# Kernel tuning notes

Hardware: AMD Instinct MI355X
Metric: run time of the kernel (lower is better)

The kernel has to match this reference:

```python
import jax, jax.numpy as jnp
import numpy as np

N = 50000        # nodes
E = 150000       # edges (avg degree ~3, chain-like RNA graphs)
F_IN = 32        # n_features
H = 32           # hidden_dim
C = 13           # n_classes
L = 3            # n_conv_layers
EDGE_HID = 10    # edge-net hidden width (Linear(2,10))
BN_EPS = 1e-5
SLOPE = 0.01     # leaky_relu default negative slope


def setup_inputs() -> dict:
    key = jax.random.key(0)
    ks = jax.random.split(key, 8)
    s = 0.1
    x = jax.random.normal(ks[0], (N, F_IN), dtype=jnp.float32)
    edge_index = jax.random.randint(ks[1], (2, E), 0, N)
    edge_attr = jax.random.uniform(ks[2], (E, 2), dtype=jnp.float32)
    # per-layer NNConv params stacked on a leading L axis (F_IN == H so all layers share shapes)
    netW1 = jax.random.normal(ks[3], (L, 2, EDGE_HID), dtype=jnp.float32) * s
    netb1 = jnp.zeros((L, EDGE_HID), dtype=jnp.float32)
    netW2 = jax.random.normal(ks[4], (L, EDGE_HID, F_IN * H), dtype=jnp.float32) * (s / np.sqrt(EDGE_HID).astype(np.float32))
    netb2 = jnp.zeros((L, F_IN * H), dtype=jnp.float32)
    root = jax.random.normal(ks[5], (L, F_IN, H), dtype=jnp.float32) * s
    conv_bias = jnp.zeros((L, H), dtype=jnp.float32)
    bn_gamma = jnp.ones((L, H), dtype=jnp.float32)
    bn_beta = jnp.zeros((L, H), dtype=jnp.float32)
    fcW = jax.random.normal(ks[6], (H, C), dtype=jnp.float32) * s
    fcb = jnp.zeros((C,), dtype=jnp.float32)
    return {"x": x, "edge_index": edge_index, "edge_attr": edge_attr,
            "netW1": netW1, "netb1": netb1, "netW2": netW2, "netb2": netb2,
            "root": root, "conv_bias": conv_bias,
            "bn_gamma": bn_gamma, "bn_beta": bn_beta, "fcW": fcW, "fcb": fcb}


def reference(x, edge_index, edge_attr, netW1, netb1, netW2, netb2, root,
              conv_bias, bn_gamma, bn_beta, fcW, fcb):
    src, dst = edge_index[0], edge_index[1]
    n = x.shape[0]
    h = x
    for i in range(L):
        # NNConv: per-edge weight matrix from edge MLP
        e = jax.nn.relu(edge_attr @ netW1[i] + netb1[i])            # [E, EDGE_HID]
        w = (e @ netW2[i] + netb2[i]).reshape(-1, h.shape[1], H)    # [E, in, H]
        m = jnp.einsum('ei,eio->eo', h[src], w)                     # messages [E, H]
        agg = jax.ops.segment_sum(m, dst, num_segments=n)           # scatter-add to targets
        h = agg + h @ root[i] + conv_bias[i]
        # BatchNorm1d (training-mode batch statistics)
        mu = h.mean(axis=0)
        var = h.var(axis=0)
        h = (h - mu) * jax.lax.rsqrt(var + BN_EPS) * bn_gamma[i] + bn_beta[i]
        # leaky_relu; dropout=0 is identity
        h = jnp.where(h > 0, h, SLOPE * h)
    logits = h @ fcW + fcb
    return jax.nn.log_softmax(logits, axis=1)
```

## Files before the change

kernel.cpp:

```cpp
#include <hip/hip_runtime.h>

#define NN 50000
#define EE 150000
#define BN_EPS 1e-5f
#define SLOPE 0.01f
#define SCAN_B 196
#define AGG_B  1563
#define MSG_B  2344

typedef __attribute__((ext_vector_type(8))) short bf16x8;
typedef __attribute__((ext_vector_type(4))) float f32x4;

__global__ __launch_bounds__(256) void k_count(const int* __restrict__ ei, int* __restrict__ cnt) {
    int e = blockIdx.x * blockDim.x + threadIdx.x;
    if (e < EE) atomicAdd(&cnt[ei[EE + e]], 1);
}

__global__ __launch_bounds__(256) void k_scanA(const int* __restrict__ cnt,
                                               int* __restrict__ rowptr,
                                               int* __restrict__ bsum) {
    __shared__ int buf[256];
    int t = threadIdx.x;
    int idx = blockIdx.x * 256 + t;
    int v = (idx <= NN) ? cnt[idx] : 0;
    buf[t] = v;
    __syncthreads();
    for (int off = 1; off < 256; off <<= 1) {
        int add = (t >= off) ? buf[t - off] : 0;
        __syncthreads();
        buf[t] += add;
        __syncthreads();
    }
    if (idx <= NN) rowptr[idx] = buf[t] - v;
    if (t == 255) bsum[blockIdx.x] = buf[255];
}

__global__ __launch_bounds__(256) void k_scanB(int* __restrict__ bsum) {
    __shared__ int buf[256];
    int t = threadIdx.x;
    int v = (t < SCAN_B) ? bsum[t] : 0;
    buf[t] = v;
    __syncthreads();
    for (int off = 1; off < 256; off <<= 1) {
        int add = (t >= off) ? buf[t - off] : 0;
        __syncthreads();
        buf[t] += add;
        __syncthreads();
    }
    if (t < SCAN_B) bsum[t] = buf[t] - v;
}

__global__ __launch_bounds__(256) void k_scanC(int* __restrict__ rowptr,
                                               int* __restrict__ cursor,
                                               const int* __restrict__ bsum) {
    int idx = blockIdx.x * 256 + threadIdx.x;
    if (idx <= NN) {
        int r = rowptr[idx] + bsum[blockIdx.x];
        rowptr[idx] = r;
        cursor[idx] = r;
    }
}

__global__ __launch_bounds__(256) void k_fill(const int* __restrict__ ei,
                                              int* __restrict__ cursor,
                                              int* __restrict__ perm) {
    int e = blockIdx.x * blockDim.x + threadIdx.x;
    if (e < EE) perm[e] = atomicAdd(&cursor[ei[EE + e]], 1);
}

__device__ __forceinline__ void bn_scsh(const float* __restrict__ stats,
                                        const float* __restrict__ gamma,
                                        const float* __restrict__ beta,
                                        int flag, float* sc, float* sh) {
    if (flag && threadIdx.x < 32) {
        int o = threadIdx.x;
        float mu = stats[o] * (1.0f / NN);
        float var = stats[32 + o] * (1.0f / NN) - mu * mu;
        float s = gamma[o] * rsqrtf(var + BN_EPS);
        sc[o] = s;
        sh[o] = fmaf(-mu, s, beta[o]);
    }
}

__global__ __launch_bounds__(256) void k_msg(
    const float* __restrict__ h, const int* __restrict__ ei,
    const float* __restrict__ ea, const float* __restrict__ W1,
    const float* __restrict__ b1, const float* __restrict__ W2,
    const float* __restrict__ b2,
    const float* __restrict__ stats, const float* __restrict__ gamma,
    const float* __restrict__ beta, int flag,
    const int* __restrict__ perm, float* __restrict__ m)
{
    __shared__ unsigned sWu[5632];
    __shared__ float hnF[2048];
    __shared__ float ekL[768];
    __shared__ float sc[32], sh[32];

    int t = threadIdx.x;
    bn_scsh(stats, gamma, beta, flag, sc, sh);
    __syncthreads();

#pragma unroll
    for (int it = 0; it < 22; ++it) {
        int idx = t + 256 * it;
        int frag = idx >> 8;
        int rem  = idx & 255;
        int lane = rem >> 2;
        int j0   = (rem & 3) * 2;
        int tile = frag & 1;
        int kstep = frag >> 1;
        int o  = tile * 16 + (lane & 15);
        int kk = kstep * 32 + (lane >> 4) * 8 + j0;
        float v0, v1;
        if (kk < 320) {
            int base = (kk >> 5) * 1024 + (kk & 31) * 32 + o;
            v0 = W2[base];
            v1 = W2[base + 32];
        } else {
            int base = (kk - 320) * 32 + o;
            v0 = b2[base];
            v1 = b2[base + 32];
        }
        sWu[idx] = __builtin_amdgcn_perm(__float_as_uint(v1), __float_as_uint(v0), 0x07060302u);
    }

    int e_loc = t & 63;
    int c     = t >> 6;
    int e_g   = blockIdx.x * 64 + e_loc;
    bool ev   = e_g < EE;

    if (c == 0) {
        float2 a = ev ? ((const float2*)ea)[e_g] : make_float2(0.f, 0.f);
#pragma unroll
        for (int k = 0; k < 10; ++k)
            ekL[e_loc * 12 + k] = fmaxf(fmaf(a.x, W1[k], fmaf(a.y, W1[10 + k], b1[k])), 0.0f);
        ekL[e_loc * 12 + 10] = 1.0f;
    }

    {
        float4 f0 = make_float4(0.f, 0.f, 0.f, 0.f);
        float4 f1 = make_float4(0.f, 0.f, 0.f, 0.f);
        if (ev) {
            int s = ei[e_g];
            f0 = *(const float4*)(h + s * 32 + c * 8);
            f1 = *(const float4*)(h + s * 32 + c * 8 + 4);
            if (flag) {
                int i0 = c * 8;
                f0.x = fmaf(f0.x, sc[i0+0], sh[i0+0]); f0.x = f0.x > 0.f ? f0.x : SLOPE*f0.x;
                f0.y = fmaf(f0.y, sc[i0+1], sh[i0+1]); f0.y = f0.y > 0.f ? f0.y : SLOPE*f0.y;
                f0.z = fmaf(f0.z, sc[i0+2], sh[i0+2]); f0.z = f0.z > 0.f ? f0.z : SLOPE*f0.z;
                f0.w = fmaf(f0.w, sc[i0+3], sh[i0+3]); f0.w = f0.w > 0.f ? f0.w : SLOPE*f0.w;
                f1.x = fmaf(f1.x, sc[i0+4], sh[i0+4]); f1.x = f1.x > 0.f ? f1.x : SLOPE*f1.x;
                f1.y = fmaf(f1.y, sc[i0+5], sh[i0+5]); f1.y = f1.y > 0.f ? f1.y : SLOPE*f1.y;
                f1.z = fmaf(f1.z, sc[i0+6], sh[i0+6]); f1.z = f1.z > 0.f ? f1.z : SLOPE*f1.z;
                f1.w = fmaf(f1.w, sc[i0+7], sh[i0+7]); f1.w = f1.w > 0.f ? f1.w : SLOPE*f1.w;
            }
        }
        int w = e_loc >> 4;
        int l = (e_loc & 15) + c * 16;
        *(float4*)&hnF[w * 512 + l * 4]       = f0;
        *(float4*)&hnF[w * 512 + 256 + l * 4] = f1;
    }
    __syncthreads();

    int lane = t & 63;
    int w    = t >> 6;
    int el   = w * 16 + (lane & 15);
    f32x4 h0 = *(const f32x4*)&hnF[w * 512 + lane * 4];
    f32x4 h1 = *(const f32x4*)&hnF[w * 512 + 256 + lane * 4];
    float ekv[11];
#pragma unroll
    for (int k = 0; k < 11; ++k) ekv[k] = ekL[el * 12 + k];

    f32x4 acc0 = {0.f, 0.f, 0.f, 0.f};
    f32x4 acc1 = {0.f, 0.f, 0.f, 0.f};
#pragma unroll
    for (int k = 0; k < 11; ++k) {
        float ekk = ekv[k];
        union { unsigned u[4]; bf16x8 v; } B;
        B.u[0] = __builtin_amdgcn_perm(__float_as_uint(ekk * h0.y), __float_as_uint(ekk * h0.x), 0x07060302u);
        B.u[1] = __builtin_amdgcn_perm(__float_as_uint(ekk * h0.w), __float_as_uint(ekk * h0.z), 0x07060302u);
        B.u[2] = __builtin_amdgcn_perm(__float_as_uint(ekk * h1.y), __float_as_uint(ekk * h1.x), 0x07060302u);
        B.u[3] = __builtin_amdgcn_perm(__float_as_uint(ekk * h1.w), __float_as_uint(ekk * h1.z), 0x07060302u);
        bf16x8 A0 = *(const bf16x8*)&sWu[(k * 2)     * 256 + lane * 4];
        bf16x8 A1 = *(const bf16x8*)&sWu[(k * 2 + 1) * 256 + lane * 4];
        acc0 = __builtin_amdgcn_mfma_f32_16x16x32_bf16(A0, B.v, acc0, 0, 0, 0);
        acc1 = __builtin_amdgcn_mfma_f32_16x16x32_bf16(A1, B.v, acc1, 0, 0, 0);
    }

    if (e_g - e_loc + el < EE) {
        int p = perm[blockIdx.x * 64 + el];
        int r = (lane >> 4) * 4;
        *(f32x4*)(m + (size_t)p * 32 + r)      = acc0;
        *(f32x4*)(m + (size_t)p * 32 + 16 + r) = acc1;
    }
}

__global__ __launch_bounds__(256) void k_agg(
    const float* __restrict__ h, const float* __restrict__ m,
    const int* __restrict__ rowptr,
    const float* __restrict__ root, const float* __restrict__ bias,
    const float* __restrict__ stats_prev, const float* __restrict__ gamma,
    const float* __restrict__ beta, int flag,
    float* __restrict__ hpre, float* __restrict__ stats_out)
{
    __shared__ float sc[32], sh[32];
    bn_scsh(stats_prev, gamma, beta, flag, sc, sh);
    __syncthreads();

    int v = blockIdx.x * 32 + (threadIdx.x >> 3);
    int cg = threadIdx.x & 7;
    float4 acc = make_float4(0.f, 0.f, 0.f, 0.f);

    if (v < NN) {
        float hn[32];
        const float4* hp = (const float4*)(h + v * 32);
#pragma unroll
        for (int q = 0; q < 8; ++q) {
            float4 t = hp[q];
            hn[4 * q] = t.x; hn[4 * q + 1] = t.y; hn[4 * q + 2] = t.z; hn[4 * q + 3] = t.w;
        }
        if (flag) {
#pragma unroll
            for (int i = 0; i < 32; ++i) {
                float y = fmaf(hn[i], sc[i], sh[i]);
                hn[i] = y > 0.f ? y : SLOPE * y;
            }
        }
        acc = ((const float4*)bias)[cg];
#pragma unroll
        for (int i = 0; i < 32; ++i) {
            float4 r = ((const float4*)(root + i * 32))[cg];
            acc.x = fmaf(hn[i], r.x, acc.x);
            acc.y = fmaf(hn[i], r.y, acc.y);
            acc.z = fmaf(hn[i], r.z, acc.z);
            acc.w = fmaf(hn[i], r.w, acc.w);
        }
        int q0 = rowptr[v], q1 = rowptr[v + 1];
        float4 acc2 = make_float4(0.f, 0.f, 0.f, 0.f);
        int p = q0;
        for (; p + 1 < q1; p += 2) {
            float4 t0 = ((const float4*)(m + (size_t)p * 32))[cg];
            float4 t1 = ((const float4*)(m + (size_t)(p + 1) * 32))[cg];
            acc.x += t0.x; acc.y += t0.y; acc.z += t0.z; acc.w += t0.w;
            acc2.x += t1.x; acc2.y += t1.y; acc2.z += t1.z; acc2.w += t1.w;
        }
        if (p < q1) {
            float4 t0 = ((const float4*)(m + (size_t)p * 32))[cg];
            acc.x += t0.x; acc.y += t0.y; acc.z += t0.z; acc.w += t0.w;
        }
        acc.x += acc2.x; acc.y += acc2.y; acc.z += acc2.z; acc.w += acc2.w;
        ((float4*)(hpre + v * 32))[cg] = acc;
    }

    float ss[8] = { acc.x, acc.y, acc.z, acc.w,
                    acc.x * acc.x, acc.y * acc.y, acc.z * acc.z, acc.w * acc.w };
#pragma unroll
    for (int d = 8; d < 64; d <<= 1) {
#pragma unroll
        for (int j = 0; j < 8; ++j) ss[j] += __shfl_xor(ss[j], d);
    }
    __shared__ float ls[2][4][8][4];
    int wave = threadIdx.x >> 6, lane = threadIdx.x & 63;
    if (lane < 8) {
#pragma unroll
        for (int j = 0; j < 4; ++j) {
            ls[0][wave][lane][j] = ss[j];
            ls[1][wave][lane][j] = ss[4 + j];
        }
    }
    __syncthreads();
    if (threadIdx.x < 64) {
        int stat = threadIdx.x >> 5, idx = threadIdx.x & 31;
        int cgg = idx >> 2, ch = idx & 3;
        float val = ls[stat][0][cgg][ch] + ls[stat][1][cgg][ch]
                  + ls[stat][2][cgg][ch] + ls[stat][3][cgg][ch];
        unsafeAtomicAdd(&stats_out[stat * 32 + idx], val);
    }
}

__global__ __launch_bounds__(256) void k_logits(const float* __restrict__ h,
                                                const float* __restrict__ fcW,
                                                const float* __restrict__ fcb,
                                                const float* __restrict__ stats,
                                                const float* __restrict__ gamma,
                                                const float* __restrict__ beta,
                                                float* __restrict__ out) {
    __shared__ float sc[32], sh[32];
    bn_scsh(stats, gamma, beta, 1, sc, sh);
    __syncthreads();

    int v = blockIdx.x * blockDim.x + threadIdx.x;
    if (v >= NN) return;
    float hv[32];
    const float4* hp = (const float4*)(h + v * 32);
#pragma unroll
    for (int q = 0; q < 8; ++q) {
        float4 t = hp[q];
        hv[4 * q] = t.x; hv[4 * q + 1] = t.y; hv[4 * q + 2] = t.z; hv[4 * q + 3] = t.w;
    }
#pragma unroll
    for (int i = 0; i < 32; ++i) {
        float y = fmaf(hv[i], sc[i], sh[i]);
        hv[i] = y > 0.f ? y : SLOPE * y;
    }
    float lg[13];
#pragma unroll
    for (int c = 0; c < 13; ++c) lg[c] = fcb[c];
#pragma unroll
    for (int i = 0; i < 32; ++i) {
        float z = hv[i];
#pragma unroll
        for (int c = 0; c < 13; ++c) lg[c] = fmaf(z, fcW[i * 13 + c], lg[c]);
    }
    float mx = lg[0];
#pragma unroll
    for (int c = 1; c < 13; ++c) mx = fmaxf(mx, lg[c]);
    float sum = 0.0f;
#pragma unroll
    for (int c = 0; c < 13; ++c) sum += expf(lg[c] - mx);
    float lse = mx + logf(sum);
#pragma unroll
    for (int c = 0; c < 13; ++c) out[v * 13 + c] = lg[c] - lse;
}

extern "C" void kernel_launch(void* const* d_in, const int* in_sizes, int n_in,
                              void* d_out, int out_size, void* d_ws, size_t ws_size,
                              hipStream_t stream) {
    const float* x     = (const float*)d_in[0];
    const int*   ei    = (const int*)  d_in[1];
    const float* ea    = (const float*)d_in[2];
    const float* netW1 = (const float*)d_in[3];
    const float* netb1 = (const float*)d_in[4];
    const float* netW2 = (const float*)d_in[5];
    const float* netb2 = (const float*)d_in[6];
    const float* root  = (const float*)d_in[7];
    const float* cbias = (const float*)d_in[8];
    const float* gamma = (const float*)d_in[9];
    const float* beta  = (const float*)d_in[10];
    const float* fcW   = (const float*)d_in[11];
    const float* fcb   = (const float*)d_in[12];
    float* out = (float*)d_out;

    char* w = (char*)d_ws;
    float* m      = (float*)(w);
    float* hA     = (float*)(w + 19200000);
    float* hB     = (float*)(w + 25600000);
    int*   rowptr = (int*)  (w + 32000000);
    int*   cursor = (int*)  (w + 32200064);
    int*   perm   = (int*)  (w + 32400128);
    float* stats  = (float*)(w + 33000128);
    int*   bsum   = (int*)  (w + 33000896);
    int*   cnt    = (int*)w;

    hipMemsetAsync(cnt, 0, (NN + 1) * sizeof(int), stream);
    hipMemsetAsync(stats, 0, 768, stream);

    k_count<<<(EE + 255) / 256, 256, 0, stream>>>(ei, cnt);
    k_scanA<<<SCAN_B, 256, 0, stream>>>(cnt, rowptr, bsum);
    k_scanB<<<1, 256, 0, stream>>>(bsum);
    k_scanC<<<SCAN_B, 256, 0, stream>>>(rowptr, cursor, bsum);
    k_fill <<<(EE + 255) / 256, 256, 0, stream>>>(ei, cursor, perm);

    const float* hcur = x;
    float* bufs[2] = { hA, hB };
    for (int i = 0; i < 3; ++i) {
        float* hnext = bufs[i & 1];
        const float* stprev = stats + (i - 1) * 64;
        k_msg<<<MSG_B, 256, 0, stream>>>(
            hcur, ei, ea, netW1 + i * 20, netb1 + i * 10,
            netW2 + i * 10240, netb2 + i * 1024,
            stprev, gamma + (i - 1) * 32, beta + (i - 1) * 32, i > 0, perm, m);
        k_agg<<<AGG_B, 256, 0, stream>>>(
            hcur, m, rowptr, root + i * 1024, cbias + i * 32,
            stprev, gamma + (i - 1) * 32, beta + (i - 1) * 32, i > 0,
            hnext, stats + i * 64);
        hcur = hnext;
    }
    k_logits<<<(NN + 255) / 256, 256, 0, stream>>>(
        hcur, fcW, fcb, stats + 2 * 64, gamma + 2 * 32, beta + 2 * 32, out);
}
```

Before: 312.3 us.

## Pre-pack edge-net weights once and drop shared-memory staging in message kernel

A new prep kernel converts each layer's W2/b2 into MFMA-fragment-ordered bf16 pairs once per call. The message kernel then reads those fragments straight from global memory instead of rebuilding a 22 KB shared tile in every block. Each lane now gathers its own source-node features and computes the edge MLP and BN scale/shift in registers, so LDS and the barriers go away. The aggregation kernel moves to 512-thread blocks with half as many blocks. In exchange, every fragment read now goes to global memory and relies on cache hits, and the BN statistics math is recomputed per lane.

```diff
diff --git a/kernel.cpp b/kernel.cpp
--- a/kernel.cpp
+++ b/kernel.cpp
@@ -5,7 +5,7 @@
 #define BN_EPS 1e-5f
 #define SLOPE 0.01f
 #define SCAN_B 196
-#define AGG_B  1563
+#define AGG_B  782
 #define MSG_B  2344
 
 typedef __attribute__((ext_vector_type(8))) short bf16x8;
@@ -66,6 +66,36 @@
                                               int* __restrict__ perm) {
     int e = blockIdx.x * blockDim.x + threadIdx.x;
     if (e < EE) perm[e] = atomicAdd(&cursor[ei[EE + e]], 1);
+}
+
+__global__ __launch_bounds__(256) void k_wprep(const float* __restrict__ netW2,
+                                               const float* __restrict__ netb2,
+                                               unsigned* __restrict__ Wfz) {
+    int layer = blockIdx.y;
+    int idx = blockIdx.x * 256 + threadIdx.x;
+    if (idx >= 5632) return;
+    const float* W2 = netW2 + layer * 10240;
+    const float* b2 = netb2 + layer * 1024;
+    int frag = idx >> 8;
+    int rem  = idx & 255;
+    int lane = rem >> 2;
+    int j0   = (rem & 3) * 2;
+    int tile = frag & 1;
+    int kstep = frag >> 1;
+    int o  = tile * 16 + (lane & 15);
+    int kk = kstep * 32 + (lane >> 4) * 8 + j0;
+    float v0, v1;
+    if (kk < 320) {
+        int base = (kk >> 5) * 1024 + (kk & 31) * 32 + o;
+        v0 = W2[base];
+        v1 = W2[base + 32];
+    } else {
+        int base = (kk - 320) * 32 + o;
+        v0 = b2[base];
+        v1 = b2[base + 32];
+    }
+    Wfz[layer * 5632 + idx] =
+        __builtin_amdgcn_perm(__float_as_uint(v1), __float_as_uint(v0), 0x07060302u);
 }
 
 __device__ __forceinline__ void bn_scsh(const float* __restrict__ stats,
@@ -85,92 +115,44 @@
 __global__ __launch_bounds__(256) void k_msg(
     const float* __restrict__ h, const int* __restrict__ ei,
     const float* __restrict__ ea, const float* __restrict__ W1,
-    const float* __restrict__ b1, const float* __restrict__ W2,
-    const float* __restrict__ b2,
+    const float* __restrict__ b1, const unsigned* __restrict__ Wfz,
     const float* __restrict__ stats, const float* __restrict__ gamma,
     const float* __restrict__ beta, int flag,
     const int* __restrict__ perm, float* __restrict__ m)
 {
-    __shared__ unsigned sWu[5632];
-    __shared__ float hnF[2048];
-    __shared__ float ekL[768];
-    __shared__ float sc[32], sh[32];
-
     int t = threadIdx.x;
-    bn_scsh(stats, gamma, beta, flag, sc, sh);
-    __syncthreads();
-
-#pragma unroll
-    for (int it = 0; it < 22; ++it) {
-        int idx = t + 256 * it;
-        int frag = idx >> 8;
-        int rem  = idx & 255;
-        int lane = rem >> 2;
-        int j0   = (rem & 3) * 2;
-        int tile = frag & 1;
-        int kstep = frag >> 1;
-        int o  = tile * 16 + (lane & 15);
-        int kk = kstep * 32 + (lane >> 4) * 8 + j0;
-        float v0, v1;
-        if (kk < 320) {
-            int base = (kk >> 5) * 1024 + (kk & 31) * 32 + o;
-            v0 = W2[base];
-            v1 = W2[base + 32];
-        } else {
-            int base = (kk - 320) * 32 + o;
-            v0 = b2[base];
-            v1 = b2[base + 32];
-        }
-        sWu[idx] = __builtin_amdgcn_perm(__float_as_uint(v1), __float_as_uint(v0), 0x07060302u);
-    }
-
-    int e_loc = t & 63;
-    int c     = t >> 6;
-    int e_g   = blockIdx.x * 64 + e_loc;
-    bool ev   = e_g < EE;
-
-    if (c == 0) {
-        float2 a = ev ? ((const float2*)ea)[e_g] : make_float2(0.f, 0.f);
-#pragma unroll
-        for (int k = 0; k < 10; ++k)
-            ekL[e_loc * 12 + k] = fmaxf(fmaf(a.x, W1[k], fmaf(a.y, W1[10 + k], b1[k])), 0.0f);
-        ekL[e_loc * 12 + 10] = 1.0f;
-    }
-
-    {
-        float4 f0 = make_float4(0.f, 0.f, 0.f, 0.f);
-        float4 f1 = make_float4(0.f, 0.f, 0.f, 0.f);
-        if (ev) {
-            int s = ei[e_g];
-            f0 = *(const float4*)(h + s * 32 + c * 8);
-            f1 = *(const float4*)(h + s * 32 + c * 8 + 4);
-            if (flag) {
-                int i0 = c * 8;
-                f0.x = fmaf(f0.x, sc[i0+0], sh[i0+0]); f0.x = f0.x > 0.f ? f0.x : SLOPE*f0.x;
-                f0.y = fmaf(f0.y, sc[i0+1], sh[i0+1]); f0.y = f0.y > 0.f ? f0.y : SLOPE*f0.y;
-                f0.z = fmaf(f0.z, sc[i0+2], sh[i0+2]); f0.z = f0.z > 0.f ? f0.z : SLOPE*f0.z;
-                f0.w = fmaf(f0.w, sc[i0+3], sh[i0+3]); f0.w = f0.w > 0.f ? f0.w : SLOPE*f0.w;
-                f1.x = fmaf(f1.x, sc[i0+4], sh[i0+4]); f1.x = f1.x > 0.f ? f1.x : SLOPE*f1.x;
-                f1.y = fmaf(f1.y, sc[i0+5], sh[i0+5]); f1.y = f1.y > 0.f ? f1.y : SLOPE*f1.y;
-                f1.z = fmaf(f1.z, sc[i0+6], sh[i0+6]); f1.z = f1.z > 0.f ? f1.z : SLOPE*f1.z;
-                f1.w = fmaf(f1.w, sc[i0+7], sh[i0+7]); f1.w = f1.w > 0.f ? f1.w : SLOPE*f1.w;
-            }
-        }
-        int w = e_loc >> 4;
-        int l = (e_loc & 15) + c * 16;
-        *(float4*)&hnF[w * 512 + l * 4]       = f0;
-        *(float4*)&hnF[w * 512 + 256 + l * 4] = f1;
-    }
-    __syncthreads();
-
     int lane = t & 63;
-    int w    = t >> 6;
-    int el   = w * 16 + (lane & 15);
-    f32x4 h0 = *(const f32x4*)&hnF[w * 512 + lane * 4];
-    f32x4 h1 = *(const f32x4*)&hnF[w * 512 + 256 + lane * 4];
+    int w = t >> 6;
+    int col = lane & 15;
+    int chunk = lane >> 4;
+    int e = blockIdx.x * 64 + w * 16 + col;
+    bool ev = e < EE;
+    int s = ev ? ei[e] : 0;
+    float2 a = ev ? ((const float2*)ea)[e] : make_float2(0.f, 0.f);
+
+    float hv[8];
+    *(float4*)&hv[0] = *(const float4*)(h + s * 32 + chunk * 8);
+    *(float4*)&hv[4] = *(const float4*)(h + s * 32 + chunk * 8 + 4);
+
+    if (flag) {
+        int i0 = chunk * 8;
+#pragma unroll
+        for (int j = 0; j < 8; ++j) {
+            int ch = i0 + j;
+            float mu = stats[ch] * (1.0f / NN);
+            float var = stats[32 + ch] * (1.0f / NN) - mu * mu;
+            float scv = gamma[ch] * rsqrtf(var + BN_EPS);
+            float shv = fmaf(-mu, scv, beta[ch]);
+            float y = fmaf(hv[j], scv, shv);
+            hv[j] = y > 0.f ? y : SLOPE * y;
+        }
+    }
+
     float ekv[11];
 #pragma unroll
-    for (int k = 0; k < 11; ++k) ekv[k] = ekL[el * 12 + k];
+    for (int k = 0; k < 10; ++k)
+        ekv[k] = fmaxf(fmaf(a.x, W1[k], fmaf(a.y, W1[10 + k], b1[k])), 0.0f);
+    ekv[10] = 1.0f;
 
     f32x4 acc0 = {0.f, 0.f, 0.f, 0.f};
     f32x4 acc1 = {0.f, 0.f, 0.f, 0.f};
@@ -178,25 +160,25 @@
     for (int k = 0; k < 11; ++k) {
         float ekk = ekv[k];
         union { unsigned u[4]; bf16x8 v; } B;
-        B.u[0] = __builtin_amdgcn_perm(__float_as_uint(ekk * h0.y), __float_as_uint(ekk * h0.x), 0x07060302u);
-        B.u[1] = __builtin_amdgcn_perm(__float_as_uint(ekk * h0.w), __float_as_uint(ekk * h0.z), 0x07060302u);
-        B.u[2] = __builtin_amdgcn_perm(__float_as_uint(ekk * h1.y), __float_as_uint(ekk * h1.x), 0x07060302u);
-        B.u[3] = __builtin_amdgcn_perm(__float_as_uint(ekk * h1.w), __float_as_uint(ekk * h1.z), 0x07060302u);
-        bf16x8 A0 = *(const bf16x8*)&sWu[(k * 2)     * 256 + lane * 4];
-        bf16x8 A1 = *(const bf16x8*)&sWu[(k * 2 + 1) * 256 + lane * 4];
+        B.u[0] = __builtin_amdgcn_perm(__float_as_uint(ekk * hv[1]), __float_as_uint(ekk * hv[0]), 0x07060302u);
+        B.u[1] = __builtin_amdgcn_perm(__float_as_uint(ekk * hv[3]), __float_as_uint(ekk * hv[2]), 0x07060302u);
+        B.u[2] = __builtin_amdgcn_perm(__float_as_uint(ekk * hv[5]), __float_as_uint(ekk * hv[4]), 0x07060302u);
+        B.u[3] = __builtin_amdgcn_perm(__float_as_uint(ekk * hv[7]), __float_as_uint(ekk * hv[6]), 0x07060302u);
+        bf16x8 A0 = *(const bf16x8*)(Wfz + (k * 2)     * 256 + lane * 4);
+        bf16x8 A1 = *(const bf16x8*)(Wfz + (k * 2 + 1) * 256 + lane * 4);
         acc0 = __builtin_amdgcn_mfma_f32_16x16x32_bf16(A0, B.v, acc0, 0, 0, 0);
         acc1 = __builtin_amdgcn_mfma_f32_16x16x32_bf16(A1, B.v, acc1, 0, 0, 0);
     }
 
-    if (e_g - e_loc + el < EE) {
-        int p = perm[blockIdx.x * 64 + el];
-        int r = (lane >> 4) * 4;
+    if (ev) {
+        int p = perm[e];
+        int r = chunk * 4;
         *(f32x4*)(m + (size_t)p * 32 + r)      = acc0;
         *(f32x4*)(m + (size_t)p * 32 + 16 + r) = acc1;
     }
 }
 
-__global__ __launch_bounds__(256) void k_agg(
+__global__ __launch_bounds__(512) void k_agg(
     const float* __restrict__ h, const float* __restrict__ m,
     const int* __restrict__ rowptr,
     const float* __restrict__ root, const float* __restrict__ bias,
@@ -208,8 +190,9 @@
     bn_scsh(stats_prev, gamma, beta, flag, sc, sh);
     __syncthreads();
 
-    int v = blockIdx.x * 32 + (threadIdx.x >> 3);
-    int cg = threadIdx.x & 7;
+    int t = threadIdx.x;
+    int v = blockIdx.x * 64 + (t >> 3);
+    int cg = t & 7;
     float4 acc = make_float4(0.f, 0.f, 0.f, 0.f);
 
     if (v < NN) {
@@ -217,8 +200,8 @@
         const float4* hp = (const float4*)(h + v * 32);
 #pragma unroll
         for (int q = 0; q < 8; ++q) {
-            float4 t = hp[q];
-            hn[4 * q] = t.x; hn[4 * q + 1] = t.y; hn[4 * q + 2] = t.z; hn[4 * q + 3] = t.w;
+            float4 tt = hp[q];
+            hn[4 * q] = tt.x; hn[4 * q + 1] = tt.y; hn[4 * q + 2] = tt.z; hn[4 * q + 3] = tt.w;
         }
         if (flag) {
 #pragma unroll
@@ -260,8 +243,8 @@
 #pragma unroll
         for (int j = 0; j < 8; ++j) ss[j] += __shfl_xor(ss[j], d);
     }
-    __shared__ float ls[2][4][8][4];
-    int wave = threadIdx.x >> 6, lane = threadIdx.x & 63;
+    __shared__ float ls[2][8][8][4];
+    int wave = t >> 6, lane = t & 63;
     if (lane < 8) {
 #pragma unroll
         for (int j = 0; j < 4; ++j) {
@@ -270,11 +253,12 @@
         }
     }
     __syncthreads();
-    if (threadIdx.x < 64) {
-        int stat = threadIdx.x >> 5, idx = threadIdx.x & 31;
+    if (t < 64) {
+        int stat = t >> 5, idx = t & 31;
         int cgg = idx >> 2, ch = idx & 3;
-        float val = ls[stat][0][cgg][ch] + ls[stat][1][cgg][ch]
-                  + ls[stat][2][cgg][ch] + ls[stat][3][cgg][ch];
+        float val = 0.f;
+#pragma unroll
+        for (int wv = 0; wv < 8; ++wv) val += ls[stat][wv][cgg][ch];
         unsafeAtomicAdd(&stats_out[stat * 32 + idx], val);
     }
 }
@@ -343,19 +327,21 @@
     float* out = (float*)d_out;
 
     char* w = (char*)d_ws;
-    float* m      = (float*)(w);
-    float* hA     = (float*)(w + 19200000);
-    float* hB     = (float*)(w + 25600000);
-    int*   rowptr = (int*)  (w + 32000000);
-    int*   cursor = (int*)  (w + 32200064);
-    int*   perm   = (int*)  (w + 32400128);
-    float* stats  = (float*)(w + 33000128);
-    int*   bsum   = (int*)  (w + 33000896);
-    int*   cnt    = (int*)w;
+    float*    m      = (float*)   (w);
+    float*    hA     = (float*)   (w + 19200000);
+    float*    hB     = (float*)   (w + 25600000);
+    int*      rowptr = (int*)     (w + 32000000);
+    int*      cursor = (int*)     (w + 32200064);
+    int*      perm   = (int*)     (w + 32400128);
+    float*    stats  = (float*)   (w + 33000128);
+    int*      bsum   = (int*)     (w + 33000896);
+    unsigned* Wfz    = (unsigned*)(w + 33001920);
+    int*      cnt    = (int*)w;
 
     hipMemsetAsync(cnt, 0, (NN + 1) * sizeof(int), stream);
     hipMemsetAsync(stats, 0, 768, stream);
 
+    k_wprep<<<dim3(22, 3), 256, 0, stream>>>(netW2, netb2, Wfz);
     k_count<<<(EE + 255) / 256, 256, 0, stream>>>(ei, cnt);
     k_scanA<<<SCAN_B, 256, 0, stream>>>(cnt, rowptr, bsum);
     k_scanB<<<1, 256, 0, stream>>>(bsum);
@@ -368,10 +354,9 @@
         float* hnext = bufs[i & 1];
         const float* stprev = stats + (i - 1) * 64;
         k_msg<<<MSG_B, 256, 0, stream>>>(
-            hcur, ei, ea, netW1 + i * 20, netb1 + i * 10,
-            netW2 + i * 10240, netb2 + i * 1024,
+            hcur, ei, ea, netW1 + i * 20, netb1 + i * 10, Wfz + i * 5632,
             stprev, gamma + (i - 1) * 32, beta + (i - 1) * 32, i > 0, perm, m);
-        k_agg<<<AGG_B, 256, 0, stream>>>(
+        k_agg<<<AGG_B, 512, 0, stream>>>(
             hcur, m, rowptr, root + i * 1024, cbias + i * 32,
             stprev, gamma + (i - 1) * 32, beta + (i - 1) * 32, i > 0,
             hnext, stats + i * 64);
```

Result: faster. 260.3 us (-16.7%).
